# Kernel optimization log

Hardware: AMD Instinct MI355X
Metric: run time of the kernel (lower is better)

The kernel has to match this reference:

```python
import jax, jax.numpy as jnp
import numpy as np

B, N, D = 4, 8192, 128
H = 4 * D  # exp_factor * features
EPS = 1e-5


def layer_norm(x):
    # fresh nn.LayerNorm each call -> weight=1, bias=0 (no learned affine)
    mu = jnp.mean(x, axis=-1, keepdims=True)
    var = jnp.var(x, axis=-1, keepdims=True)
    return (x - mu) * jax.lax.rsqrt(var + EPS)


def setup_inputs() -> dict:
    key = jax.random.key(0)
    ks = jax.random.split(key, 8)
    x = jax.random.normal(ks[0], (B, N, D), dtype=jnp.float32)
    adj = jax.random.uniform(ks[1], (N, N), dtype=jnp.float32)
    attn_mask = jnp.ones((1,), dtype=jnp.int32)  # unused (torch masked_fill result discarded)
    pad_mask = jnp.ones((1,), dtype=jnp.int32)   # unused
    # FFN params (torch Linear default init scale ~ 1/sqrt(fan_in))
    w1 = jax.random.normal(ks[2], (D, H), dtype=jnp.float32) / np.sqrt(D)
    b1 = jnp.zeros((H,), dtype=jnp.float32)
    w2 = jax.random.normal(ks[3], (H, D), dtype=jnp.float32) / np.sqrt(H)
    b2 = jnp.zeros((D,), dtype=jnp.float32)
    return {"x": x, "adj": adj, "attn_mask": attn_mask, "pad_mask": pad_mask,
            "w1": w1, "b1": b1, "w2": w2, "b2": b2, "dim": 128}


def reference(x, adj, attn_mask, pad_mask, w1, b1, w2, b2, dim):
    # Sublayer 0: x + InrAwaSA(LN(x))
    h = layer_norm(x)                               # [B,N,D]
    # adj is provided -> scores = dense adj, shared across batch.
    # NOTE: masks are no-ops in the source (masked_fill not in-place).
    prob = jax.nn.softmax(adj, axis=-1)             # [N,N]
    attn_out = jnp.einsum('nm,bmd->bnd', prob, h)   # [B,N,D]
    x1 = x + attn_out
    # Sublayer 1: x1 + FFN(LN(x1))
    h1 = layer_norm(x1)
    ffn = jnp.maximum(h1 @ w1 + b1, 0.0) @ w2 + b2
    return x1 + ffn
```

## Files before the change

### kernel.cpp

```cpp
#include <hip/hip_runtime.h>
#include <hip/hip_bf16.h>

typedef __attribute__((ext_vector_type(8))) short bh8;
typedef __attribute__((ext_vector_type(4))) float fx4;
typedef __attribute__((ext_vector_type(8))) int i32x8;
typedef __attribute__((ext_vector_type(4))) int i32x4;

typedef const __attribute__((address_space(1))) unsigned int* gas_p;
typedef __attribute__((address_space(3))) unsigned int* las_p;

#define MFMA(a, b, c) __builtin_amdgcn_mfma_f32_16x16x32_bf16((a), (b), (c), 0, 0, 0)
#define MFMAS(a, b, c) __builtin_amdgcn_mfma_scale_f32_16x16x128_f8f6f4( \
    (a), (b), (c), 0, 0, 0, 0x7f7f7f7f, 0, 0x7f7f7f7f)

__device__ __forceinline__ unsigned short f2bf(float f) {
  unsigned u = __builtin_bit_cast(unsigned, f);
  u += 0x7fff + ((u >> 16) & 1);
  return (unsigned short)(u >> 16);
}

__device__ __forceinline__ float bflo2f(unsigned u) { return __builtin_bit_cast(float, u << 16); }

__device__ __forceinline__ void gld16(const void* g, void* l) {
  __builtin_amdgcn_global_load_lds((gas_p)g, (las_p)l, 16, 0, 0);
}

__global__ __launch_bounds__(256) void transpose_weights(const float* __restrict__ w1,
                                                         const float* __restrict__ w2,
                                                         unsigned short* __restrict__ w1t,
                                                         unsigned short* __restrict__ w2t) {
  const int tgl = blockIdx.x * 256 + threadIdx.x;
  { const int h = tgl >> 7, d = tgl & 127; w1t[tgl] = f2bf(w1[d * 512 + h]); }
  { const int d = tgl >> 9, h = tgl & 511; w2t[tgl] = f2bf(w2[h * 128 + d]); }
}

__global__ __launch_bounds__(256) void ln1_transpose(const float* __restrict__ x,
                                                     unsigned char* __restrict__ htf) {
  const int t = threadIdx.x, lane = t & 63, w = t >> 6;
  const int mt = blockIdx.x, b = blockIdx.y;
  __shared__ unsigned short tile[128 * 64];
  const float* xb = x + ((size_t)b * 8192 + (size_t)mt * 64) * 128;
  for (int it = 0; it < 16; ++it) {
    const int r = w * 16 + it;
    const float2 v = *(const float2*)(xb + r * 128 + lane * 2);
    float s = v.x + v.y, s2 = v.x * v.x + v.y * v.y;
    #pragma unroll
    for (int o = 1; o < 64; o <<= 1) { s += __shfl_xor(s, o); s2 += __shfl_xor(s2, o); }
    const float mean = s * 0.0078125f;
    const float var = s2 * 0.0078125f - mean * mean;
    const float rstd = rsqrtf(var + 1e-5f);
    const int mc = r >> 3, ml = r & 7;
    const int d0 = lane * 2, d1 = d0 + 1;
    tile[d0 * 64 + ((mc ^ (d0 & 7)) << 3) + ml] = f2bf((v.x - mean) * rstd);
    tile[d1 * 64 + ((mc ^ (d1 & 7)) << 3) + ml] = f2bf((v.y - mean) * rstd);
  }
  __syncthreads();
  #pragma unroll
  for (int i = 0; i < 4; ++i) {
    const int idx = i * 256 + t;
    const int d = idx >> 3, mc = idx & 7;
    const bh8 vv = *(const bh8*)(tile + d * 64 + ((mc ^ (d & 7)) << 3));
    int lo = 0, hi = 0;
    lo = __builtin_amdgcn_cvt_pk_fp8_f32(bflo2f((unsigned short)vv[0]),
                                         bflo2f((unsigned short)vv[1]), lo, false);
    lo = __builtin_amdgcn_cvt_pk_fp8_f32(bflo2f((unsigned short)vv[2]),
                                         bflo2f((unsigned short)vv[3]), lo, true);
    hi = __builtin_amdgcn_cvt_pk_fp8_f32(bflo2f((unsigned short)vv[4]),
                                         bflo2f((unsigned short)vv[5]), hi, false);
    hi = __builtin_amdgcn_cvt_pk_fp8_f32(bflo2f((unsigned short)vv[6]),
                                         bflo2f((unsigned short)vv[7]), hi, true);
    const int col = b * 128 + d;
    const int k0 = mt * 64 + mc * 8;
    const int frag = (k0 >> 7) * 32 + (col >> 4);
    const int off = ((col & 15) + 16 * ((k0 >> 5) & 3)) * 32 + (k0 & 31);
    *(uint2*)(htf + (size_t)frag * 2048 + off) = (uint2){(unsigned)lo, (unsigned)hi};
  }
}

__global__ __launch_bounds__(256, 2) void fused_attn(const float* __restrict__ adj,
                                                     const unsigned char* __restrict__ htf,
                                                     unsigned short* __restrict__ pbuf,
                                                     float* __restrict__ sden) {
  const int tid = threadIdx.x, lane = tid & 63, wn = tid >> 6;
  const int mt = blockIdx.x, z = blockIdx.y;
  const int kbase = z * 2048;

  __shared__ unsigned char Al[64 * 128];

  fx4 acc[4][8];
  #pragma unroll
  for (int i = 0; i < 4; ++i)
    #pragma unroll
    for (int j = 0; j < 8; ++j) acc[i][j] = (fx4){0.f, 0.f, 0.f, 0.f};

  i32x8 afr[4];

  const int ar = tid >> 2, aq = tid & 3;
  const float* aroot = adj + (size_t)(mt * 64 + ar) * 8192 + kbase;
  float sacc = 0.f;
  float4 a4[8];
  unsigned pk[8];

  auto issueAdj = [&](int tau) {
    #pragma unroll
    for (int j = 0; j < 8; ++j)
      a4[j] = *(const float4*)(aroot + tau * 128 + aq * 32 + j * 4);
  };
  auto expCvt = [&]() {
    #pragma unroll
    for (int j = 0; j < 8; ++j) {
      const float e0 = __expf(a4[j].x), e1 = __expf(a4[j].y);
      const float e2 = __expf(a4[j].z), e3 = __expf(a4[j].w);
      sacc += (e0 + e1) + (e2 + e3);
      int d = 0;
      d = __builtin_amdgcn_cvt_pk_fp8_f32(e0, e1, d, false);
      d = __builtin_amdgcn_cvt_pk_fp8_f32(e2, e3, d, true);
      pk[j] = (unsigned)d;
    }
  };
  auto writeA = [&]() {
    const i32x4 w0 = (i32x4){(int)pk[0], (int)pk[1], (int)pk[2], (int)pk[3]};
    const i32x4 w1 = (i32x4){(int)pk[4], (int)pk[5], (int)pk[6], (int)pk[7]};
    *(i32x4*)&Al[ar * 128 + (((aq * 2) ^ (ar & 7)) << 4)] = w0;
    *(i32x4*)&Al[ar * 128 + (((aq * 2 + 1) ^ (ar & 7)) << 4)] = w1;
  };
  auto ldAall = [&]() {
    #pragma unroll
    for (int mf = 0; mf < 4; ++mf) {
      const int rr = mf * 16 + (lane & 15);
      const int gb = (lane >> 4) * 2;
      const unsigned char* base = &Al[rr * 128];
      const i32x4 lo = *(const i32x4*)(base + ((gb ^ (rr & 7)) << 4));
      const i32x4 hi = *(const i32x4*)(base + (((gb + 1) ^ (rr & 7)) << 4));
      afr[mf] = (i32x8){lo.x, lo.y, lo.z, lo.w, hi.x, hi.y, hi.z, hi.w};
    }
  };

  issueAdj(0);
  expCvt();
  writeA();
  asm volatile("s_waitcnt lgkmcnt(0)" ::: "memory");
  __builtin_amdgcn_sched_barrier(0);
  __builtin_amdgcn_s_barrier();
  __builtin_amdgcn_sched_barrier(0);

  for (int tt = 0; tt < 16; ++tt) {
    ldAall();
    if (tt < 15) issueAdj(tt + 1);

    const int gkt = z * 16 + tt;
    const unsigned char* fb = htf + ((size_t)gkt * 32 + wn * 8) * 2048 + lane * 32;
    #pragma unroll
    for (int nf = 0; nf < 8; ++nf) {
      const unsigned char* fp = fb + nf * 2048;
      const i32x4 blo = *(const i32x4*)(fp);
      const i32x4 bhi = *(const i32x4*)(fp + 16);
      const i32x8 bfr = (i32x8){blo.x, blo.y, blo.z, blo.w, bhi.x, bhi.y, bhi.z, bhi.w};
      #pragma unroll
      for (int mf = 0; mf < 4; ++mf)
        acc[mf][nf] = MFMAS(afr[mf], bfr, acc[mf][nf]);
    }

    asm volatile("s_waitcnt lgkmcnt(0)" ::: "memory");
    __builtin_amdgcn_sched_barrier(0);
    __builtin_amdgcn_s_barrier();
    __builtin_amdgcn_sched_barrier(0);

    if (tt < 15) {
      expCvt();
      writeA();
      asm volatile("s_waitcnt lgkmcnt(0)" ::: "memory");
      __builtin_amdgcn_sched_barrier(0);
      __builtin_amdgcn_s_barrier();
      __builtin_amdgcn_sched_barrier(0);
    }
  }

  sacc += __shfl_xor(sacc, 1);
  sacc += __shfl_xor(sacc, 2);
  if (aq == 0) sden[(size_t)z * 8192 + mt * 64 + ar] = sacc;

  unsigned short* po = pbuf + (size_t)z * 8192 * 512;
  #pragma unroll
  for (int mf = 0; mf < 4; ++mf)
    #pragma unroll
    for (int nf = 0; nf < 8; ++nf) {
      const int col = wn * 128 + nf * 16 + (lane & 15);
      #pragma unroll
      for (int q = 0; q < 4; ++q) {
        const int row = mt * 64 + mf * 16 + (lane >> 4) * 4 + q;
        po[(size_t)row * 512 + col] = f2bf(acc[mf][nf][q]);
      }
    }
}

#define SWZ16(ks, r) (((((ks) & 7) ^ ((r) & 7)) | ((ks) & 8)))
__global__ __launch_bounds__(512) void ln_ffn_kernel(const float* __restrict__ x,
                                                     const unsigned short* __restrict__ pbuf,
                                                     const float* __restrict__ sden,
                                                     const unsigned short* __restrict__ w1t,
                                                     const unsigned short* __restrict__ w2t,
                                                     const float* __restrict__ b1,
                                                     const float* __restrict__ b2,
                                                     float* __restrict__ out) {
  const int t = threadIdx.x, lane = t & 63, w = t >> 6;
  const int wr = w >> 1, wc = w & 1;
  const int row0 = blockIdx.x * 128;
  __shared__ unsigned short As[128 * 128];
  __shared__ unsigned short W1c[128 * 128];
  __shared__ unsigned short W2c[128 * 128];
  __shared__ unsigned short Ts[128 * 128];

  auto stageW1 = [&](int hc) {
    #pragma unroll
    for (int i = 0; i < 4; ++i) {
      const int idx = i * 512 + t;
      const int row = idx >> 4, kc = idx & 15;
      const int kcs = (kc & 8) | ((kc & 7) ^ (row & 7));
      gld16(w1t + (size_t)(hc * 128 + row) * 128 + kcs * 8, W1c + (idx & ~63) * 8);
    }
  };
  auto stageW2 = [&](int hc) {
    #pragma unroll
    for (int i = 0; i < 4; ++i) {
      const int idx = i * 512 + t;
      const int row = idx >> 4, kc = idx & 15;
      const int kcs = (kc & 8) | ((kc & 7) ^ (row & 7));
      gld16(w2t + (size_t)row * 512 + hc * 128 + kcs * 8, W2c + (idx & ~63) * 8);
    }
  };

  stageW1(0); stageW2(0);

  const int r = t >> 2, q = t & 3, c0 = q * 32;
  const int rowg = row0 + r;
  const int bb = rowg >> 13, nn = rowg & 8191;
  float xv[32];
  {
    const float den = sden[nn] + sden[8192 + nn] + sden[16384 + nn] + sden[24576 + nn];
    const float rinv = 1.f / den;
    const float* xp = x + (size_t)rowg * 128 + c0;
    #pragma unroll
    for (int j = 0; j < 8; ++j) {
      const float4 v4 = *(const float4*)(xp + 4 * j);
      xv[4 * j] = v4.x; xv[4 * j + 1] = v4.y; xv[4 * j + 2] = v4.z; xv[4 * j + 3] = v4.w;
    }
    #pragma unroll
    for (int z = 0; z < 4; ++z) {
      const unsigned short* pp = pbuf + ((size_t)z * 8192 + nn) * 512 + bb * 128 + c0;
      #pragma unroll
      for (int j = 0; j < 4; ++j) {
        const bh8 pv = *(const bh8*)(pp + 8 * j);
        #pragma unroll
        for (int e = 0; e < 8; ++e) xv[8 * j + e] += bflo2f((unsigned short)pv[e]) * rinv;
      }
    }
  }
  float s = 0.f, s2 = 0.f;
  #pragma unroll
  for (int j = 0; j < 32; ++j) { s += xv[j]; s2 += xv[j] * xv[j]; }
  s += __shfl_xor(s, 1); s2 += __shfl_xor(s2, 1);
  s += __shfl_xor(s, 2); s2 += __shfl_xor(s2, 2);
  const float mean = s * 0.0078125f;
  const float var = s2 * 0.0078125f - mean * mean;
  const float rstd = rsqrtf(var + 1e-5f);
  #pragma unroll
  for (int j = 0; j < 4; ++j) {
    const int g = q * 4 + j;
    bh8 pk;
    #pragma unroll
    for (int e = 0; e < 8; ++e) pk[e] = (short)f2bf((xv[8 * j + e] - mean) * rstd);
    *(bh8*)(As + r * 128 + SWZ16(g, r) * 8) = pk;
  }
  __syncthreads();

  fx4 accO[2][4];
  #pragma unroll
  for (int i = 0; i < 2; ++i)
    #pragma unroll
    for (int j = 0; j < 4; ++j) accO[i][j] = (fx4){0.f, 0.f, 0.f, 0.f};

  for (int hc = 0; hc < 4; ++hc) {
    if (hc > 0) stageW2(hc);
    fx4 accT[2][4];
    #pragma unroll
    for (int i = 0; i < 2; ++i)
      #pragma unroll
      for (int j = 0; j < 4; ++j) accT[i][j] = (fx4){0.f, 0.f, 0.f, 0.f};
    #pragma unroll
    for (int kk = 0; kk < 4; ++kk) {
      const int ks = kk * 4 + (lane >> 4);
      bh8 af[2], bfr[4];
      #pragma unroll
      for (int f = 0; f < 2; ++f) {
        const int ra = wr * 32 + f * 16 + (lane & 15);
        af[f] = *(const bh8*)(As + ra * 128 + SWZ16(ks, ra) * 8);
      }
      #pragma unroll
      for (int f = 0; f < 4; ++f) {
        const int rb = wc * 64 + f * 16 + (lane & 15);
        bfr[f] = *(const bh8*)(W1c + rb * 128 + SWZ16(ks, rb) * 8);
      }
      #pragma unroll
      for (int fm = 0; fm < 2; ++fm)
        #pragma unroll
        for (int fn = 0; fn < 4; ++fn) accT[fm][fn] = MFMA(af[fm], bfr[fn], accT[fm][fn]);
    }
    #pragma unroll
    for (int fm = 0; fm < 2; ++fm)
      #pragma unroll
      for (int fn = 0; fn < 4; ++fn) {
        const int col = wc * 64 + fn * 16 + (lane & 15);
        const float bv = b1[hc * 128 + col];
        const int c = col >> 3;
        #pragma unroll
        for (int qq = 0; qq < 4; ++qq) {
          const int row = wr * 32 + fm * 16 + (lane >> 4) * 4 + qq;
          float vv = accT[fm][fn][qq] + bv;
          vv = fmaxf(vv, 0.f);
          Ts[row * 128 + SWZ16(c, row) * 8 + (col & 7)] = f2bf(vv);
        }
      }
    __syncthreads();
    if (hc < 3) {
      stageW1(hc + 1);
    } else {
      float* dst = (r < 64) ? (float*)As + r * 128 + c0 : (float*)W1c + (r - 64) * 128 + c0;
      #pragma unroll
      for (int j = 0; j < 8; ++j)
        *(float4*)(dst + 4 * j) =
            (float4){xv[4 * j], xv[4 * j + 1], xv[4 * j + 2], xv[4 * j + 3]};
    }
    #pragma unroll
    for (int kk = 0; kk < 4; ++kk) {
      const int ks = kk * 4 + (lane >> 4);
      bh8 af[2], bfr[4];
      #pragma unroll
      for (int f = 0; f < 2; ++f) {
        const int ra = wr * 32 + f * 16 + (lane & 15);
        af[f] = *(const bh8*)(Ts + ra * 128 + SWZ16(ks, ra) * 8);
      }
      #pragma unroll
      for (int f = 0; f < 4; ++f) {
        const int rb = wc * 64 + f * 16 + (lane & 15);
        bfr[f] = *(const bh8*)(W2c + rb * 128 + SWZ16(ks, rb) * 8);
      }
      #pragma unroll
      for (int fm = 0; fm < 2; ++fm)
        #pragma unroll
        for (int fn = 0; fn < 4; ++fn) accO[fm][fn] = MFMA(af[fm], bfr[fn], accO[fm][fn]);
    }
    __syncthreads();
  }

  const float* x1a = (const float*)As;
  const float* x1b = (const float*)W1c;
  float* op = out + (size_t)row0 * 128;
  #pragma unroll
  for (int fm = 0; fm < 2; ++fm)
    #pragma unroll
    for (int fn = 0; fn < 4; ++fn) {
      const int col = wc * 64 + fn * 16 + (lane & 15);
      const float bv = b2[col];
      #pragma unroll
      for (int qq = 0; qq < 4; ++qq) {
        const int row = wr * 32 + fm * 16 + (lane >> 4) * 4 + qq;
        const float x1v = (row < 64) ? x1a[row * 128 + col] : x1b[(row - 64) * 128 + col];
        op[row * 128 + col] = x1v + accO[fm][fn][qq] + bv;
      }
    }
}

extern "C" void kernel_launch(void* const* d_in, const int* in_sizes, int n_in,
                              void* d_out, int out_size, void* d_ws, size_t ws_size,
                              hipStream_t stream) {
  const float* x   = (const float*)d_in[0];
  const float* adj = (const float*)d_in[1];
  const float* w1  = (const float*)d_in[4];
  const float* b1  = (const float*)d_in[5];
  const float* w2  = (const float*)d_in[6];
  const float* b2  = (const float*)d_in[7];
  float* out = (float*)d_out;

  char* p = (char*)d_ws;
  unsigned short* w1t  = (unsigned short*)p; p += (size_t)512 * 128 * 2;
  unsigned short* w2t  = (unsigned short*)p; p += (size_t)128 * 512 * 2;
  unsigned char*  htf  = (unsigned char*)p;  p += (size_t)4 * 128 * 8192;
  unsigned short* pbuf = (unsigned short*)p; p += (size_t)4 * 8192 * 512 * 2;
  float*          sden = (float*)p;          p += (size_t)4 * 8192 * 4;

  transpose_weights<<<256, 256, 0, stream>>>(w1, w2, w1t, w2t);
  ln1_transpose<<<dim3(128, 4), 256, 0, stream>>>(x, htf);
  fused_attn<<<dim3(128, 4), 256, 0, stream>>>(adj, htf, pbuf, sden);
  ln_ffn_kernel<<<256, 512, 0, stream>>>(x, pbuf, sden, w1t, w2t, b1, b2, out);
}
```

Baseline: 162.9 us.

## Warp-specialize fused attention into producer exp waves and consumer MFMA waves

The fused attention block now runs 512 threads. Four producer waves load adj, compute exp, pack it to fp8 and write a double-buffered LDS tile. Four consumer waves read that tile and run the fp8 MFMAs against the transposed h fragments. This is meant to overlap the exp/convert and global adj loads with the matrix math instead of running them in sequence within each wave. It also changes the A-tile LDS layout into fragment-ready order, which drops the swizzle. The trade-offs are one block per CU instead of two, and barrier-count coupling between the two wave roles.

Measured after the change: 181.7 us. +11.6%, slower.

```diff
diff --git a/kernel.cpp b/kernel.cpp
--- a/kernel.cpp
+++ b/kernel.cpp
@@ -77,121 +77,130 @@
   }
 }
 
-__global__ __launch_bounds__(256, 2) void fused_attn(const float* __restrict__ adj,
+__global__ __launch_bounds__(512, 1) void fused_attn(const float* __restrict__ adj,
                                                      const unsigned char* __restrict__ htf,
                                                      unsigned short* __restrict__ pbuf,
                                                      float* __restrict__ sden) {
-  const int tid = threadIdx.x, lane = tid & 63, wn = tid >> 6;
+  const int tid = threadIdx.x, lane = tid & 63, w = tid >> 6;
   const int mt = blockIdx.x, z = blockIdx.y;
   const int kbase = z * 2048;
 
-  __shared__ unsigned char Al[64 * 128];
-
-  fx4 acc[4][8];
-  #pragma unroll
-  for (int i = 0; i < 4; ++i)
-    #pragma unroll
-    for (int j = 0; j < 8; ++j) acc[i][j] = (fx4){0.f, 0.f, 0.f, 0.f};
-
-  i32x8 afr[4];
-
-  const int ar = tid >> 2, aq = tid & 3;
-  const float* aroot = adj + (size_t)(mt * 64 + ar) * 8192 + kbase;
-  float sacc = 0.f;
-  float4 a4[8];
-  unsigned pk[8];
-
-  auto issueAdj = [&](int tau) {
-    #pragma unroll
-    for (int j = 0; j < 8; ++j)
-      a4[j] = *(const float4*)(aroot + tau * 128 + aq * 32 + j * 4);
-  };
-  auto expCvt = [&]() {
-    #pragma unroll
-    for (int j = 0; j < 8; ++j) {
-      const float e0 = __expf(a4[j].x), e1 = __expf(a4[j].y);
-      const float e2 = __expf(a4[j].z), e3 = __expf(a4[j].w);
-      sacc += (e0 + e1) + (e2 + e3);
-      int d = 0;
-      d = __builtin_amdgcn_cvt_pk_fp8_f32(e0, e1, d, false);
-      d = __builtin_amdgcn_cvt_pk_fp8_f32(e2, e3, d, true);
-      pk[j] = (unsigned)d;
-    }
-  };
-  auto writeA = [&]() {
-    const i32x4 w0 = (i32x4){(int)pk[0], (int)pk[1], (int)pk[2], (int)pk[3]};
-    const i32x4 w1 = (i32x4){(int)pk[4], (int)pk[5], (int)pk[6], (int)pk[7]};
-    *(i32x4*)&Al[ar * 128 + (((aq * 2) ^ (ar & 7)) << 4)] = w0;
-    *(i32x4*)&Al[ar * 128 + (((aq * 2 + 1) ^ (ar & 7)) << 4)] = w1;
-  };
-  auto ldAall = [&]() {
-    #pragma unroll
-    for (int mf = 0; mf < 4; ++mf) {
-      const int rr = mf * 16 + (lane & 15);
-      const int gb = (lane >> 4) * 2;
-      const unsigned char* base = &Al[rr * 128];
-      const i32x4 lo = *(const i32x4*)(base + ((gb ^ (rr & 7)) << 4));
-      const i32x4 hi = *(const i32x4*)(base + (((gb + 1) ^ (rr & 7)) << 4));
-      afr[mf] = (i32x8){lo.x, lo.y, lo.z, lo.w, hi.x, hi.y, hi.z, hi.w};
-    }
-  };
-
-  issueAdj(0);
-  expCvt();
-  writeA();
-  asm volatile("s_waitcnt lgkmcnt(0)" ::: "memory");
-  __builtin_amdgcn_sched_barrier(0);
-  __builtin_amdgcn_s_barrier();
-  __builtin_amdgcn_sched_barrier(0);
-
-  for (int tt = 0; tt < 16; ++tt) {
-    ldAall();
-    if (tt < 15) issueAdj(tt + 1);
-
-    const int gkt = z * 16 + tt;
-    const unsigned char* fb = htf + ((size_t)gkt * 32 + wn * 8) * 2048 + lane * 32;
-    #pragma unroll
-    for (int nf = 0; nf < 8; ++nf) {
-      const unsigned char* fp = fb + nf * 2048;
-      const i32x4 blo = *(const i32x4*)(fp);
-      const i32x4 bhi = *(const i32x4*)(fp + 16);
-      const i32x8 bfr = (i32x8){blo.x, blo.y, blo.z, blo.w, bhi.x, bhi.y, bhi.z, bhi.w};
-      #pragma unroll
-      for (int mf = 0; mf < 4; ++mf)
-        acc[mf][nf] = MFMAS(afr[mf], bfr, acc[mf][nf]);
-    }
-
+  __shared__ unsigned char Al[2][8192];
+
+  if (w < 4) {
+    const int pw = w;
+    const int row = (lane & 15), kq = lane >> 4;
+    const float* aroot = adj + (size_t)(mt * 64 + pw * 16 + row) * 8192 + kbase + kq * 32;
+    float sacc = 0.f;
+    float4 a4a[8], a4b[8];
+    unsigned pk[8];
+
+    auto issueP = [&](float4 (&dst)[8], int tau) {
+      #pragma unroll
+      for (int j = 0; j < 8; ++j)
+        dst[j] = *(const float4*)(aroot + tau * 128 + j * 4);
+    };
+    auto expCvt = [&](const float4 (&src)[8]) {
+      #pragma unroll
+      for (int j = 0; j < 8; ++j) {
+        const float e0 = __expf(src[j].x), e1 = __expf(src[j].y);
+        const float e2 = __expf(src[j].z), e3 = __expf(src[j].w);
+        sacc += (e0 + e1) + (e2 + e3);
+        int d = 0;
+        d = __builtin_amdgcn_cvt_pk_fp8_f32(e0, e1, d, false);
+        d = __builtin_amdgcn_cvt_pk_fp8_f32(e2, e3, d, true);
+        pk[j] = (unsigned)d;
+      }
+    };
+    auto writeAl = [&](int buf) {
+      unsigned char* base = &Al[buf][pw * 2048];
+      *(i32x4*)(base + lane * 16) =
+          (i32x4){(int)pk[0], (int)pk[1], (int)pk[2], (int)pk[3]};
+      *(i32x4*)(base + 1024 + lane * 16) =
+          (i32x4){(int)pk[4], (int)pk[5], (int)pk[6], (int)pk[7]};
+    };
+
+    issueP(a4a, 0);
+    issueP(a4b, 1);
+    expCvt(a4a);
+    writeAl(0);
     asm volatile("s_waitcnt lgkmcnt(0)" ::: "memory");
     __builtin_amdgcn_sched_barrier(0);
     __builtin_amdgcn_s_barrier();
     __builtin_amdgcn_sched_barrier(0);
 
-    if (tt < 15) {
-      expCvt();
-      writeA();
+    #pragma unroll 1
+    for (int i = 0; i < 8; ++i) {
+      const int te = 2 * i;
+      if (te + 2 < 16) issueP(a4a, te + 2);
+      if (te + 1 < 16) { expCvt(a4b); writeAl(1); }
       asm volatile("s_waitcnt lgkmcnt(0)" ::: "memory");
       __builtin_amdgcn_sched_barrier(0);
       __builtin_amdgcn_s_barrier();
       __builtin_amdgcn_sched_barrier(0);
-    }
-  }
-
-  sacc += __shfl_xor(sacc, 1);
-  sacc += __shfl_xor(sacc, 2);
-  if (aq == 0) sden[(size_t)z * 8192 + mt * 64 + ar] = sacc;
-
-  unsigned short* po = pbuf + (size_t)z * 8192 * 512;
-  #pragma unroll
-  for (int mf = 0; mf < 4; ++mf)
-    #pragma unroll
-    for (int nf = 0; nf < 8; ++nf) {
-      const int col = wn * 128 + nf * 16 + (lane & 15);
-      #pragma unroll
-      for (int q = 0; q < 4; ++q) {
-        const int row = mt * 64 + mf * 16 + (lane >> 4) * 4 + q;
-        po[(size_t)row * 512 + col] = f2bf(acc[mf][nf][q]);
-      }
-    }
+      const int to = te + 1;
+      if (to + 2 < 16) issueP(a4b, to + 2);
+      if (to + 1 < 16) { expCvt(a4a); writeAl(0); }
+      asm volatile("s_waitcnt lgkmcnt(0)" ::: "memory");
+      __builtin_amdgcn_sched_barrier(0);
+      __builtin_amdgcn_s_barrier();
+      __builtin_amdgcn_sched_barrier(0);
+    }
+
+    sacc += __shfl_xor(sacc, 16);
+    sacc += __shfl_xor(sacc, 32);
+    if (kq == 0) sden[(size_t)z * 8192 + mt * 64 + pw * 16 + row] = sacc;
+  } else {
+    const int cn = w - 4;
+    fx4 acc[4][8];
+    #pragma unroll
+    for (int a = 0; a < 4; ++a)
+      #pragma unroll
+      for (int b = 0; b < 8; ++b) acc[a][b] = (fx4){0.f, 0.f, 0.f, 0.f};
+
+    __builtin_amdgcn_s_barrier();
+    __builtin_amdgcn_sched_barrier(0);
+
+    #pragma unroll 1
+    for (int tt = 0; tt < 16; ++tt) {
+      i32x8 afr[4];
+      const unsigned char* ab = &Al[tt & 1][0];
+      #pragma unroll
+      for (int mf = 0; mf < 4; ++mf) {
+        const i32x4 lo = *(const i32x4*)(ab + mf * 2048 + lane * 16);
+        const i32x4 hi = *(const i32x4*)(ab + mf * 2048 + 1024 + lane * 16);
+        afr[mf] = (i32x8){lo.x, lo.y, lo.z, lo.w, hi.x, hi.y, hi.z, hi.w};
+      }
+      const int gkt = z * 16 + tt;
+      const unsigned char* fb = htf + ((size_t)gkt * 32 + cn * 8) * 2048 + lane * 32;
+      #pragma unroll
+      for (int nf = 0; nf < 8; ++nf) {
+        const i32x4 blo = *(const i32x4*)(fb + nf * 2048);
+        const i32x4 bhi = *(const i32x4*)(fb + nf * 2048 + 16);
+        const i32x8 bfr = (i32x8){blo.x, blo.y, blo.z, blo.w, bhi.x, bhi.y, bhi.z, bhi.w};
+        #pragma unroll
+        for (int mf = 0; mf < 4; ++mf)
+          acc[mf][nf] = MFMAS(afr[mf], bfr, acc[mf][nf]);
+      }
+      asm volatile("s_waitcnt lgkmcnt(0)" ::: "memory");
+      __builtin_amdgcn_sched_barrier(0);
+      __builtin_amdgcn_s_barrier();
+      __builtin_amdgcn_sched_barrier(0);
+    }
+
+    unsigned short* po = pbuf + (size_t)z * 8192 * 512;
+    #pragma unroll
+    for (int mf = 0; mf < 4; ++mf)
+      #pragma unroll
+      for (int nf = 0; nf < 8; ++nf) {
+        const int col = cn * 128 + nf * 16 + (lane & 15);
+        #pragma unroll
+        for (int q = 0; q < 4; ++q) {
+          const int row = mt * 64 + mf * 16 + (lane >> 4) * 4 + q;
+          po[(size_t)row * 512 + col] = f2bf(acc[mf][nf][q]);
+        }
+      }
+  }
 }
 
 #define SWZ16(ks, r) (((((ks) & 7) ^ ((r) & 7)) | ((ks) & 8)))
@@ -391,6 +400,6 @@
 
   transpose_weights<<<256, 256, 0, stream>>>(w1, w2, w1t, w2t);
   ln1_transpose<<<dim3(128, 4), 256, 0, stream>>>(x, htf);
-  fused_attn<<<dim3(128, 4), 256, 0, stream>>>(adj, htf, pbuf, sden);
+  fused_attn<<<dim3(128, 4), 512, 0, stream>>>(adj, htf, pbuf, sden);
   ln_ffn_kernel<<<256, 512, 0, stream>>>(x, pbuf, sden, w1t, w2t, b1, b2, out);
 }
```
